# Kernel tuning notes

Measured on AMD Instinct MI355X. Metric: run time of the kernel, lower is better.

The kernel has to match this reference:

```python
import jax, jax.numpy as jnp
import numpy as np

MARGIN = 1.0


def setup_inputs() -> dict:
    key = jax.random.key(0)
    k1, k2, k3 = jax.random.split(key, 3)
    B, P = 8192, 16
    return {
        "energies": jax.random.normal(k1, (B, 1), dtype=jnp.float32),
        "property_values": jax.random.normal(k2, (B, P), dtype=jnp.float32),
        "property_targets": jax.random.normal(k3, (P,), dtype=jnp.float32),
    }


def reference(energies, property_values, property_targets):
    # distances[i] = ||property_values[i] - property_targets||_2, shape [B]
    distances = jnp.linalg.norm(property_values - property_targets[None, :], axis=-1)
    B = energies.shape[0]
    e = energies[:, 0]  # [B]
    # pair mask: i != j and distances[i] < distances[j]  -> [B, B]
    mask = (distances[:, None] < distances[None, :]) & (~jnp.eye(B, dtype=bool))
    # ranking loss per pair: relu(e_i - e_j + margin)
    pair_loss = jax.nn.relu(e[:, None] - e[None, :] + MARGIN)
    loss_sum = jnp.sum(jnp.where(mask, pair_loss, 0.0))
    count = jnp.sum(mask).astype(jnp.float32)
    loss = loss_sum / jnp.maximum(count, 1.0)
    # torch version accumulates [1]-shaped tensors -> output shape [1]
    return loss[None]
```

## Files before the change

kernel.cpp:

```cpp
#include <hip/hip_runtime.h>
#include <math.h>

#define MARGIN 1.0f
#define NI 16

__global__ __launch_bounds__(256) void dist_kernel(
    const float* __restrict__ pv,
    const float* __restrict__ pt,
    float* __restrict__ dist,
    int B, int P)
{
    int i = blockIdx.x * 256 + threadIdx.x;
    if (i >= B) return;
    const float* row = pv + (size_t)i * P;
    float s = 0.f;
    if (P == 16) {
        const float4* r4 = (const float4*)row;
        const float4* t4 = (const float4*)pt;
        #pragma unroll
        for (int q = 0; q < 4; ++q) {
            float4 r = r4[q], t = t4[q];
            float d0 = r.x - t.x; s = fmaf(d0, d0, s);
            float d1 = r.y - t.y; s = fmaf(d1, d1, s);
            float d2 = r.z - t.z; s = fmaf(d2, d2, s);
            float d3 = r.w - t.w; s = fmaf(d3, d3, s);
        }
    } else {
        for (int p = 0; p < P; ++p) { float d = row[p] - pt[p]; s = fmaf(d, d, s); }
    }
    dist[i] = sqrtf(s);
}

__global__ __launch_bounds__(256) void pair_kernel(
    const float* __restrict__ e,
    const float* __restrict__ dist,
    float* __restrict__ psum,
    float* __restrict__ pcnt,
    int B)
{
    const int tid = threadIdx.x;
    const int i0 = blockIdx.x * NI;

    float di[NI], ai[NI];
    #pragma unroll
    for (int ii = 0; ii < NI; ++ii) {
        const int i = i0 + ii;
        const bool iok = i < B;
        di[ii] = iok ? dist[i] : INFINITY;
        ai[ii] = iok ? (e[i] + MARGIN) : 0.f;
    }

    float s0 = 0.f, s1 = 0.f, s2 = 0.f, s3 = 0.f;
    unsigned c0 = 0u, c1 = 0u, c2 = 0u, c3 = 0u;

    auto proc = [&](float dj, float ej) {
        #pragma unroll
        for (int ii = 0; ii < NI; ii += 4) {
            { const bool m = di[ii]   < dj; const float t = fmaxf(ai[ii]   - ej, 0.f); s0 += m ? t : 0.f; c0 += (unsigned)m; }
            { const bool m = di[ii+1] < dj; const float t = fmaxf(ai[ii+1] - ej, 0.f); s1 += m ? t : 0.f; c1 += (unsigned)m; }
            { const bool m = di[ii+2] < dj; const float t = fmaxf(ai[ii+2] - ej, 0.f); s2 += m ? t : 0.f; c2 += (unsigned)m; }
            { const bool m = di[ii+3] < dj; const float t = fmaxf(ai[ii+3] - ej, 0.f); s3 += m ? t : 0.f; c3 += (unsigned)m; }
        }
    };

    const int nvec = B >> 2;
    const float4* d4 = (const float4*)dist;
    const float4* e4 = (const float4*)e;

    const int nfull = nvec >> 8;
    float4 dc, ec;
    if (nfull > 0) { dc = d4[tid]; ec = e4[tid]; }
    for (int s = 0; s < nfull; ++s) {
        float4 dn, en;
        const bool more = (s + 1) < nfull;
        const int jn = ((s + 1) << 8) + tid;
        if (more) { dn = d4[jn]; en = e4[jn]; }
        proc(dc.x, ec.x);
        proc(dc.y, ec.y);
        proc(dc.z, ec.z);
        proc(dc.w, ec.w);
        if (more) { dc = dn; ec = en; }
    }
    for (int j4 = (nfull << 8) + tid; j4 < nvec; j4 += 256) {
        const float4 dv = d4[j4], ev = e4[j4];
        proc(dv.x, ev.x); proc(dv.y, ev.y); proc(dv.z, ev.z); proc(dv.w, ev.w);
    }
    for (int j = (nvec << 2) + tid; j < B; j += 256) {
        proc(dist[j], e[j]);
    }

    float sum = (s0 + s1) + (s2 + s3);
    float cnt = (float)((c0 + c1) + (c2 + c3));
    #pragma unroll
    for (int o = 32; o > 0; o >>= 1) {
        sum += __shfl_xor(sum, o);
        cnt += __shfl_xor(cnt, o);
    }

    __shared__ float rs[4], rc[4];
    const int wid = tid >> 6;
    if ((tid & 63) == 0) { rs[wid] = sum; rc[wid] = cnt; }
    __syncthreads();
    if (tid == 0) {
        psum[blockIdx.x] = (rs[0] + rs[1]) + (rs[2] + rs[3]);
        pcnt[blockIdx.x] = (rc[0] + rc[1]) + (rc[2] + rc[3]);
    }
}

__global__ __launch_bounds__(256) void finalize_kernel(
    const float* __restrict__ psum,
    const float* __restrict__ pcnt,
    float* __restrict__ out,
    int nblk)
{
    __shared__ double ss[256];
    __shared__ double sc[256];
    double s = 0.0, c = 0.0;
    for (int k = threadIdx.x; k < nblk; k += 256) {
        s += (double)psum[k];
        c += (double)pcnt[k];
    }
    ss[threadIdx.x] = s;
    sc[threadIdx.x] = c;
    __syncthreads();
    for (int st = 128; st > 0; st >>= 1) {
        if ((int)threadIdx.x < st) {
            ss[threadIdx.x] += ss[threadIdx.x + st];
            sc[threadIdx.x] += sc[threadIdx.x + st];
        }
        __syncthreads();
    }
    if (threadIdx.x == 0) {
        double cnt = sc[0] < 1.0 ? 1.0 : sc[0];
        out[0] = (float)(ss[0] / cnt);
    }
}

extern "C" void kernel_launch(void* const* d_in, const int* in_sizes, int n_in,
                              void* d_out, int out_size, void* d_ws, size_t ws_size,
                              hipStream_t stream)
{
    const float* energies = (const float*)d_in[0];
    const float* pv       = (const float*)d_in[1];
    const float* pt       = (const float*)d_in[2];
    int B = in_sizes[0];
    int P = in_sizes[2];

    int nblk = (B + NI - 1) / NI;

    float* dist = (float*)d_ws;
    float* psum = dist + B;
    float* pcnt = psum + nblk;

    dist_kernel<<<(B + 255) / 256, 256, 0, stream>>>(pv, pt, dist, B, P);
    pair_kernel<<<nblk, 256, 0, stream>>>(energies, dist, psum, pcnt, B);
    finalize_kernel<<<1, 256, 0, stream>>>(psum, pcnt, (float*)d_out, nblk);
}
```

Baseline: 71.17 us.

## Fuse distance computation into pair kernel, recomputing column distances per block

Removes the separate distance kernel. Each block computes its own row distances into shared memory and recomputes every column distance on the fly from the raw property rows. The tile also grows to 32 rows and 512 threads per block, which halves the number of blocks. This drops one launch and the distance buffer round-trip, but every block now reads the full 512 KB property matrix instead of a 32 KB distance array, adding L2 traffic and about 16 FMAs per column.

```diff
diff --git a/kernel.cpp b/kernel.cpp
--- a/kernel.cpp
+++ b/kernel.cpp
@@ -2,53 +2,51 @@
 #include <math.h>
 
 #define MARGIN 1.0f
-#define NI 16
+#define NI 32
+#define BT 512
 
-__global__ __launch_bounds__(256) void dist_kernel(
+__global__ __launch_bounds__(BT) void pairdist_kernel(
+    const float* __restrict__ e,
     const float* __restrict__ pv,
     const float* __restrict__ pt,
-    float* __restrict__ dist,
+    float* __restrict__ psum,
+    float* __restrict__ pcnt,
     int B, int P)
 {
-    int i = blockIdx.x * 256 + threadIdx.x;
-    if (i >= B) return;
-    const float* row = pv + (size_t)i * P;
-    float s = 0.f;
-    if (P == 16) {
-        const float4* r4 = (const float4*)row;
-        const float4* t4 = (const float4*)pt;
-        #pragma unroll
-        for (int q = 0; q < 4; ++q) {
-            float4 r = r4[q], t = t4[q];
-            float d0 = r.x - t.x; s = fmaf(d0, d0, s);
-            float d1 = r.y - t.y; s = fmaf(d1, d1, s);
-            float d2 = r.z - t.z; s = fmaf(d2, d2, s);
-            float d3 = r.w - t.w; s = fmaf(d3, d3, s);
+    const int tid = threadIdx.x;
+    const int i0  = blockIdx.x * NI;
+
+    __shared__ float sdi[NI], sai[NI];
+    if (tid < NI) {
+        const int i = i0 + tid;
+        float dv = INFINITY, av = 0.f;
+        if (i < B) {
+            const float* row = pv + (size_t)i * P;
+            float s = 0.f;
+            if (P == 16) {
+                const float4* r4 = (const float4*)row;
+                const float4* t4 = (const float4*)pt;
+                #pragma unroll
+                for (int q = 0; q < 4; ++q) {
+                    float4 r = r4[q], t = t4[q];
+                    float d0 = r.x - t.x; s = fmaf(d0, d0, s);
+                    float d1 = r.y - t.y; s = fmaf(d1, d1, s);
+                    float d2 = r.z - t.z; s = fmaf(d2, d2, s);
+                    float d3 = r.w - t.w; s = fmaf(d3, d3, s);
+                }
+            } else {
+                for (int p = 0; p < P; ++p) { float d = row[p] - pt[p]; s = fmaf(d, d, s); }
+            }
+            dv = sqrtf(s);
+            av = e[i] + MARGIN;
         }
-    } else {
-        for (int p = 0; p < P; ++p) { float d = row[p] - pt[p]; s = fmaf(d, d, s); }
+        sdi[tid] = dv; sai[tid] = av;
     }
-    dist[i] = sqrtf(s);
-}
-
-__global__ __launch_bounds__(256) void pair_kernel(
-    const float* __restrict__ e,
-    const float* __restrict__ dist,
-    float* __restrict__ psum,
-    float* __restrict__ pcnt,
-    int B)
-{
-    const int tid = threadIdx.x;
-    const int i0 = blockIdx.x * NI;
+    __syncthreads();
 
     float di[NI], ai[NI];
     #pragma unroll
-    for (int ii = 0; ii < NI; ++ii) {
-        const int i = i0 + ii;
-        const bool iok = i < B;
-        di[ii] = iok ? dist[i] : INFINITY;
-        ai[ii] = iok ? (e[i] + MARGIN) : 0.f;
-    }
+    for (int ii = 0; ii < NI; ++ii) { di[ii] = sdi[ii]; ai[ii] = sai[ii]; }
 
     float s0 = 0.f, s1 = 0.f, s2 = 0.f, s3 = 0.f;
     unsigned c0 = 0u, c1 = 0u, c2 = 0u, c3 = 0u;
@@ -63,30 +61,63 @@
         }
     };
 
-    const int nvec = B >> 2;
-    const float4* d4 = (const float4*)dist;
-    const float4* e4 = (const float4*)e;
+    if (P == 16) {
+        const float4 t0 = ((const float4*)pt)[0];
+        const float4 t1 = ((const float4*)pt)[1];
+        const float4 t2 = ((const float4*)pt)[2];
+        const float4 t3 = ((const float4*)pt)[3];
 
-    const int nfull = nvec >> 8;
-    float4 dc, ec;
-    if (nfull > 0) { dc = d4[tid]; ec = e4[tid]; }
-    for (int s = 0; s < nfull; ++s) {
-        float4 dn, en;
-        const bool more = (s + 1) < nfull;
-        const int jn = ((s + 1) << 8) + tid;
-        if (more) { dn = d4[jn]; en = e4[jn]; }
-        proc(dc.x, ec.x);
-        proc(dc.y, ec.y);
-        proc(dc.z, ec.z);
-        proc(dc.w, ec.w);
-        if (more) { dc = dn; ec = en; }
-    }
-    for (int j4 = (nfull << 8) + tid; j4 < nvec; j4 += 256) {
-        const float4 dv = d4[j4], ev = e4[j4];
-        proc(dv.x, ev.x); proc(dv.y, ev.y); proc(dv.z, ev.z); proc(dv.w, ev.w);
-    }
-    for (int j = (nvec << 2) + tid; j < B; j += 256) {
-        proc(dist[j], e[j]);
+        auto dist_of = [&](float4 r0, float4 r1, float4 r2, float4 r3) {
+            float s = 0.f, d;
+            d = r0.x - t0.x; s = fmaf(d, d, s);
+            d = r0.y - t0.y; s = fmaf(d, d, s);
+            d = r0.z - t0.z; s = fmaf(d, d, s);
+            d = r0.w - t0.w; s = fmaf(d, d, s);
+            d = r1.x - t1.x; s = fmaf(d, d, s);
+            d = r1.y - t1.y; s = fmaf(d, d, s);
+            d = r1.z - t1.z; s = fmaf(d, d, s);
+            d = r1.w - t1.w; s = fmaf(d, d, s);
+            d = r2.x - t2.x; s = fmaf(d, d, s);
+            d = r2.y - t2.y; s = fmaf(d, d, s);
+            d = r2.z - t2.z; s = fmaf(d, d, s);
+            d = r2.w - t2.w; s = fmaf(d, d, s);
+            d = r3.x - t3.x; s = fmaf(d, d, s);
+            d = r3.y - t3.y; s = fmaf(d, d, s);
+            d = r3.z - t3.z; s = fmaf(d, d, s);
+            d = r3.w - t3.w; s = fmaf(d, d, s);
+            return sqrtf(s);
+        };
+
+        const int nfull = B / BT;
+        float4 r0, r1, r2, r3; float ejc;
+        if (nfull > 0) {
+            const float4* row = (const float4*)(pv + (size_t)tid * 16);
+            r0 = row[0]; r1 = row[1]; r2 = row[2]; r3 = row[3];
+            ejc = e[tid];
+        }
+        for (int s = 0; s < nfull; ++s) {
+            float4 n0, n1, n2, n3; float ejn;
+            const bool more = (s + 1) < nfull;
+            if (more) {
+                const int jn = (s + 1) * BT + tid;
+                const float4* row = (const float4*)(pv + (size_t)jn * 16);
+                n0 = row[0]; n1 = row[1]; n2 = row[2]; n3 = row[3];
+                ejn = e[jn];
+            }
+            proc(dist_of(r0, r1, r2, r3), ejc);
+            if (more) { r0 = n0; r1 = n1; r2 = n2; r3 = n3; ejc = ejn; }
+        }
+        for (int j = nfull * BT + tid; j < B; j += BT) {
+            const float4* row = (const float4*)(pv + (size_t)j * 16);
+            proc(dist_of(row[0], row[1], row[2], row[3]), e[j]);
+        }
+    } else {
+        for (int j = tid; j < B; j += BT) {
+            const float* row = pv + (size_t)j * P;
+            float s = 0.f;
+            for (int p = 0; p < P; ++p) { float d = row[p] - pt[p]; s = fmaf(d, d, s); }
+            proc(sqrtf(s), e[j]);
+        }
     }
 
     float sum = (s0 + s1) + (s2 + s3);
@@ -97,13 +128,16 @@
         cnt += __shfl_xor(cnt, o);
     }
 
-    __shared__ float rs[4], rc[4];
+    __shared__ float rs[BT / 64], rc[BT / 64];
     const int wid = tid >> 6;
     if ((tid & 63) == 0) { rs[wid] = sum; rc[wid] = cnt; }
     __syncthreads();
     if (tid == 0) {
-        psum[blockIdx.x] = (rs[0] + rs[1]) + (rs[2] + rs[3]);
-        pcnt[blockIdx.x] = (rc[0] + rc[1]) + (rc[2] + rc[3]);
+        float S = 0.f, C = 0.f;
+        #pragma unroll
+        for (int w = 0; w < BT / 64; ++w) { S += rs[w]; C += rc[w]; }
+        psum[blockIdx.x] = S;
+        pcnt[blockIdx.x] = C;
     }
 }
 
@@ -148,11 +182,9 @@
 
     int nblk = (B + NI - 1) / NI;
 
-    float* dist = (float*)d_ws;
-    float* psum = dist + B;
+    float* psum = (float*)d_ws;
     float* pcnt = psum + nblk;
 
-    dist_kernel<<<(B + 255) / 256, 256, 0, stream>>>(pv, pt, dist, B, P);
-    pair_kernel<<<nblk, 256, 0, stream>>>(energies, dist, psum, pcnt, B);
+    pairdist_kernel<<<nblk, BT, 0, stream>>>(energies, pv, pt, psum, pcnt, B, P);
     finalize_kernel<<<1, 256, 0, stream>>>(psum, pcnt, (float*)d_out, nblk);
 }
```

Measured after the change: 76.15 us. +7.0%, slower.
